# Optimization experiments

Hardware: AMD Instinct MI355X
Metric: run time of the kernel (lower is better)

The kernel has to match this reference:

```python
import jax, jax.numpy as jnp
import numpy as np

N_EMBD = 1024
N_HEAD = 16
DIM_HEAD = N_EMBD // N_HEAD
SCALE = DIM_HEAD ** (-0.5)  # source divides by this (i.e. multiplies scores by sqrt(dim_head))


def setup_inputs() -> dict:
    key = jax.random.key(0)
    k1, k2, k3, k4, k5 = jax.random.split(key, 5)
    B, Tq, Tkv = 2, 2048, 2048
    x_q = jax.random.normal(k1, (B, Tq, N_EMBD), dtype=jnp.float32)
    x_kv = jax.random.normal(k2, (B, Tkv, N_EMBD), dtype=jnp.float32)
    s = 0.02
    W_q = jax.random.normal(k3, (N_EMBD, N_EMBD), dtype=jnp.float32) * s
    W_kv = jax.random.normal(k4, (N_EMBD, 2 * N_EMBD), dtype=jnp.float32) * s
    W_proj = jax.random.normal(k5, (N_EMBD, N_EMBD), dtype=jnp.float32) * s
    return {"x_q": x_q, "x_kv": x_kv, "W_q": W_q, "W_kv": W_kv, "W_proj": W_proj}


def reference(x_q, x_kv, W_q, W_kv, W_proj):
    B, Tq, C = x_q.shape
    Tkv = x_kv.shape[1]
    q = x_q @ W_q                      # [B, Tq, C]
    kv = x_kv @ W_kv                   # [B, Tkv, 2C]
    k, v = jnp.split(kv, 2, axis=2)
    # [B, H, T, Dh]
    q = q.reshape(B, Tq, N_HEAD, DIM_HEAD).transpose(0, 2, 1, 3)
    k = k.reshape(B, Tkv, N_HEAD, DIM_HEAD).transpose(0, 2, 1, 3)
    v = v.reshape(B, Tkv, N_HEAD, DIM_HEAD).transpose(0, 2, 1, 3)
    # Faithful to source: scores = q@k^T / scale  (== * sqrt(dim_head))
    attn = jnp.einsum('bhqd,bhkd->bhqk', q, k) / SCALE
    attn = jax.nn.softmax(attn, axis=-1)
    y = jnp.einsum('bhqk,bhkd->bhqd', attn, v)
    y = y.transpose(0, 2, 1, 3).reshape(B, Tq, C)
    return y @ W_proj
```

## Files before the change

kernel.cpp:

```cpp
#include <hip/hip_runtime.h>
#include <cstddef>

typedef _Float16 f16;
typedef _Float16 f16x8 __attribute__((ext_vector_type(8)));
typedef _Float16 f16x4 __attribute__((ext_vector_type(4)));
typedef _Float16 f16x2 __attribute__((ext_vector_type(2)));
typedef float f32x4 __attribute__((ext_vector_type(4)));
typedef float f32x16 __attribute__((ext_vector_type(16)));
typedef unsigned int u32;

__device__ inline float exp2_fast(float x) {
  float r;
  asm("v_exp_f32 %0, %1" : "=v"(r) : "v"(x));
  return r;
}

__device__ inline int pk2(float x, float y) {
  return __builtin_bit_cast(int, __builtin_amdgcn_cvt_pkrtz(x, y));
}

__device__ inline f16x2 pk2h(float x, float y) {
  return __builtin_bit_cast(f16x2, __builtin_amdgcn_cvt_pkrtz(x, y));
}

__device__ inline void permlane32_swap(int& a, int& b) {
  asm volatile("v_permlane32_swap_b32 %0, %1" : "+v"(a), "+v"(b));
}

__global__ __launch_bounds__(256) void prep(
    const float* __restrict__ xq, const float* __restrict__ xkv,
    f16* __restrict__ oq, f16* __restrict__ okv,
    const float* __restrict__ Wq, const float* __restrict__ Wkv,
    const float* __restrict__ Wp, f16* __restrict__ Wqt,
    f16* __restrict__ Wkvt, f16* __restrict__ Wpt) {
  __shared__ float t[32][33];
  int bid = blockIdx.x;
  if (bid < 8192) {
    const float* in = (bid < 4096) ? xq : xkv;
    f16* out = (bid < 4096) ? oq : okv;
    int i = ((bid & 4095) * 256 + threadIdx.x) * 4;
    float4 v = *(const float4*)&in[i];
    f16x4 h;
    h[0] = (f16)v.x; h[1] = (f16)v.y; h[2] = (f16)v.z; h[3] = (f16)v.w;
    *(f16x4*)&out[i] = h;
  } else {
    int zz = bid - 8192;
    int bx = zz & 31, by = (zz >> 5) & 31, z = zz >> 10;
    const float* in;
    f16* out;
    int N = 1024, extra = 0;
    if (z == 0) { in = Wq; out = Wqt; }
    else if (z == 3) { in = Wp; out = Wpt; }
    else { in = Wkv; out = Wkvt; N = 2048; extra = (z - 1) * 1024; }
    int tx = threadIdx.x % 32, ty = threadIdx.x / 32;
    int n0 = bx * 32 + extra, k0 = by * 32;
#pragma unroll
    for (int i = 0; i < 32; i += 8)
      t[ty + i][tx] = in[(size_t)(k0 + ty + i) * N + n0 + tx];
    __syncthreads();
#pragma unroll
    for (int i = 0; i < 32; i += 8)
      out[(size_t)(n0 + ty + i) * 1024 + k0 + tx] = (f16)t[tx][ty + i];
  }
}

template <int BN, typename CT>
__device__ __forceinline__ void gemm_body(
    const f16* __restrict__ A, const f16* __restrict__ Bt, CT* __restrict__ C,
    int bid, int M, int N, int K, float scale, f16* As, f16* Bs) {
  constexpr int NT = BN / 32;
  constexpr int BI = BN / 32;
  const int nb = N / BN;
  const int m0 = (bid / nb) * 128;
  const int n0 = (bid % nb) * BN;
  const int tid = threadIdx.x;
  const int w = tid >> 6, lane = tid & 63;
  const int l16 = lane & 15, quad = lane >> 4;
  const int wrow = (w >> 1) * 64, wcol = (w & 1) * (BN / 2);
  const int sr = tid >> 3, sc8 = tid & 7;
  const int wc8 = sc8 ^ (sr & 7);

  f32x4 acc[4][NT] = {};
  f16x8 ar[4], br[BI];

#pragma unroll
  for (int i = 0; i < 4; i++)
    ar[i] = *(const f16x8*)&A[(size_t)(m0 + sr + i * 32) * K + sc8 * 8];
#pragma unroll
  for (int i = 0; i < BI; i++)
    br[i] = *(const f16x8*)&Bt[(size_t)(n0 + sr + i * 32) * K + sc8 * 8];

  for (int k0 = 0; k0 < K; k0 += 64) {
#pragma unroll
    for (int i = 0; i < 4; i++)
      *(f16x8*)&As[(sr + i * 32) * 64 + wc8 * 8] = ar[i];
#pragma unroll
    for (int i = 0; i < BI; i++)
      *(f16x8*)&Bs[(sr + i * 32) * 64 + wc8 * 8] = br[i];
    __syncthreads();

    if (k0 + 64 < K) {
#pragma unroll
      for (int i = 0; i < 4; i++)
        ar[i] = *(const f16x8*)&A[(size_t)(m0 + sr + i * 32) * K + k0 + 64 + sc8 * 8];
#pragma unroll
      for (int i = 0; i < BI; i++)
        br[i] = *(const f16x8*)&Bt[(size_t)(n0 + sr + i * 32) * K + k0 + 64 + sc8 * 8];
    }

    f16x8 bf[NT][2];
#pragma unroll
    for (int nt = 0; nt < NT; nt++) {
      const int row = wcol + nt * 16 + l16;
#pragma unroll
      for (int s = 0; s < 2; s++)
        bf[nt][s] = *(const f16x8*)&Bs[row * 64 + (((s * 4 + quad) ^ (row & 7)) << 3)];
    }
#pragma unroll
    for (int mt = 0; mt < 4; mt++) {
      const int row = wrow + mt * 16 + l16;
      f16x8 af0 = *(const f16x8*)&As[row * 64 + ((quad ^ (row & 7)) << 3)];
      f16x8 af1 = *(const f16x8*)&As[row * 64 + (((4 + quad) ^ (row & 7)) << 3)];
#pragma unroll
      for (int nt = 0; nt < NT; nt++) {
        acc[mt][nt] = __builtin_amdgcn_mfma_f32_16x16x32_f16(af0, bf[nt][0], acc[mt][nt], 0, 0, 0);
        acc[mt][nt] = __builtin_amdgcn_mfma_f32_16x16x32_f16(af1, bf[nt][1], acc[mt][nt], 0, 0, 0);
      }
    }
    __syncthreads();
  }

#pragma unroll
  for (int mt = 0; mt < 4; mt++)
#pragma unroll
    for (int nt = 0; nt < NT; nt++)
#pragma unroll
      for (int r = 0; r < 4; r++) {
        int row = m0 + wrow + mt * 16 + quad * 4 + r;
        int col = n0 + wcol + nt * 16 + l16;
        C[(size_t)row * N + col] = (CT)(acc[mt][nt][r] * scale);
      }
}

__global__ __launch_bounds__(256, 3) void qkv_gemm(
    const f16* __restrict__ Xq, const f16* __restrict__ Wqt, f16* __restrict__ Qh,
    const f16* __restrict__ Xkv, const f16* __restrict__ Wkvt, f16* __restrict__ KVh,
    float sc_q) {
  __shared__ f16 As[128 * 64];
  __shared__ f16 Bs[128 * 64];
  if (blockIdx.x < 256)
    gemm_body<128, f16>(Xq, Wqt, Qh, blockIdx.x, 4096, 1024, 1024, sc_q, As, Bs);
  else
    gemm_body<128, f16>(Xkv, Wkvt, KVh, blockIdx.x - 256, 4096, 2048, 1024, 1.0f, As, Bs);
}

template <int BN, typename CT>
__global__ __launch_bounds__(256, 2) void gemm_lds(
    const f16* __restrict__ A, const f16* __restrict__ Bt, CT* __restrict__ C,
    int M, int N, int K, float scale) {
  __shared__ f16 As[128 * 64];
  __shared__ f16 Bs[BN * 64];
  gemm_body<BN, CT>(A, Bt, C, blockIdx.x, M, N, K, scale, As, Bs);
}

__global__ __launch_bounds__(256) void attn_kernel(
    const f16* __restrict__ Qh, const f16* __restrict__ KVh, f16* __restrict__ Yh) {
  __shared__ f16 smem[9216];
  f16* Ks = smem;
  f16* Vt = smem + 64 * 72;

  const int bid = blockIdx.x;
  const int hb = bid & 31;
  const int qt = bid >> 5;
  const int h = hb >> 1, b = hb & 1;
  const int tid = threadIdx.x;
  const int w = tid >> 6, lane = tid & 63;
  const int l31 = lane & 31, e = lane >> 5;

  const size_t qrow0 = (size_t)b * 2048 + (size_t)qt * 128;
  const size_t kvrow0 = (size_t)b * 2048;

  f16x8 qf[4];
#pragma unroll
  for (int ks = 0; ks < 4; ks++)
    qf[ks] = *(const f16x8*)&Qh[(qrow0 + w * 32 + l31) * 1024 + h * 64 + ks * 16 + e * 8];

  float m_run = -1e30f, l_run = 0.0f;
  f32x16 o_acc[2] = {};

  const int ksr = tid >> 2, ksc = (tid & 3) << 4;
  const int vkv0 = (tid >> 3) * 2;
  const int vd0 = (tid & 7) * 8;
  const int vcol = ((((vkv0 >> 3) ^ (tid & 7)) << 3) | (vkv0 & 7));

  f16x8 kr0, kr1, vr0, vr1;
  {
    const f16* kb = &KVh[(kvrow0 + ksr) * 2048 + h * 64 + ksc];
    kr0 = *(const f16x8*)kb;
    kr1 = *(const f16x8*)(kb + 8);
    const f16* vb = &KVh[(kvrow0 + vkv0) * 2048 + 1024 + h * 64 + vd0];
    vr0 = *(const f16x8*)vb;
    vr1 = *(const f16x8*)(vb + 2048);
  }

  for (int t = 0; t < 32; t++) {
    *(f16x8*)&Ks[ksr * 72 + ksc] = kr0;
    *(f16x8*)&Ks[ksr * 72 + ksc + 8] = kr1;
#pragma unroll
    for (int j = 0; j < 8; j++) {
      f16x2 p; p[0] = vr0[j]; p[1] = vr1[j];
      *(f16x2*)&Vt[(vd0 + j) * 72 + vcol] = p;
    }
    __syncthreads();

    if (t + 1 < 32) {
      const f16* kb = &KVh[(kvrow0 + (t + 1) * 64 + ksr) * 2048 + h * 64 + ksc];
      kr0 = *(const f16x8*)kb;
      kr1 = *(const f16x8*)(kb + 8);
      const f16* vb = &KVh[(kvrow0 + (t + 1) * 64 + vkv0) * 2048 + 1024 + h * 64 + vd0];
      vr0 = *(const f16x8*)vb;
      vr1 = *(const f16x8*)(vb + 2048);
    }

    f32x16 sacc[2] = {};
#pragma unroll
    for (int kvt = 0; kvt < 2; kvt++)
#pragma unroll
      for (int ks = 0; ks < 4; ks++) {
        f16x8 a = *(const f16x8*)&Ks[(kvt * 32 + l31) * 72 + ks * 16 + e * 8];
        sacc[kvt] = __builtin_amdgcn_mfma_f32_32x32x16_f16(a, qf[ks], sacc[kvt], 0, 0, 0);
      }

    float mxa[4];
#pragma unroll
    for (int j = 0; j < 4; j++) {
      float a = fmaxf(fmaxf(sacc[0][j], sacc[0][j + 4]),
                      fmaxf(sacc[0][j + 8], sacc[0][j + 12]));
      float bb = fmaxf(fmaxf(sacc[1][j], sacc[1][j + 4]),
                       fmaxf(sacc[1][j + 8], sacc[1][j + 12]));
      mxa[j] = fmaxf(a, bb);
    }
    float mx = fmaxf(fmaxf(mxa[0], mxa[1]), fmaxf(mxa[2], mxa[3]));
    mx = fmaxf(mx, __shfl_xor(mx, 32, 64));

    if (!__all(mx <= m_run + 8.0f)) {
      float mnew = fmaxf(m_run, mx);
      float alpha = exp2_fast(m_run - mnew);
      m_run = mnew;
      l_run *= alpha;
#pragma unroll
      for (int r = 0; r < 16; r++) { o_acc[0][r] *= alpha; o_acc[1][r] *= alpha; }
    }

    float ss0 = 0.0f, ss1 = 0.0f, ss2 = 0.0f, ss3 = 0.0f;
#pragma unroll
    for (int kvt = 0; kvt < 2; kvt++)
#pragma unroll
      for (int r = 0; r < 16; r += 4) {
        float p0 = exp2_fast(sacc[kvt][r + 0] - m_run);
        float p1 = exp2_fast(sacc[kvt][r + 1] - m_run);
        float p2 = exp2_fast(sacc[kvt][r + 2] - m_run);
        float p3 = exp2_fast(sacc[kvt][r + 3] - m_run);
        sacc[kvt][r + 0] = p0; sacc[kvt][r + 1] = p1;
        sacc[kvt][r + 2] = p2; sacc[kvt][r + 3] = p3;
        ss0 += p0; ss1 += p1; ss2 += p2; ss3 += p3;
      }
    float ssum = (ss0 + ss1) + (ss2 + ss3);
    ssum += __shfl_xor(ssum, 32, 64);
    l_run += ssum;

    f16x8 pf[4];
#pragma unroll
    for (int kvt = 0; kvt < 2; kvt++)
#pragma unroll
      for (int half = 0; half < 2; half++) {
        const int h8 = half * 8;
        int a0 = pk2(sacc[kvt][h8 + 0], sacc[kvt][h8 + 1]);
        int b0 = pk2(sacc[kvt][h8 + 4], sacc[kvt][h8 + 5]);
        int a1 = pk2(sacc[kvt][h8 + 2], sacc[kvt][h8 + 3]);
        int b1 = pk2(sacc[kvt][h8 + 6], sacc[kvt][h8 + 7]);
        permlane32_swap(a0, b0);
        permlane32_swap(a1, b1);
        union { int i[4]; f16x8 v; } u;
        u.i[0] = a0; u.i[1] = a1; u.i[2] = b0; u.i[3] = b1;
        pf[kvt * 2 + half] = u.v;
      }

#pragma unroll
    for (int dt = 0; dt < 2; dt++) {
      const int d = dt * 32 + l31;
      const int dx = d >> 3;
#pragma unroll
      for (int ks = 0; ks < 4; ks++) {
        f16x8 va = *(const f16x8*)&Vt[d * 72 + (((ks * 2 + e) ^ dx) << 3)];
        o_acc[dt] = __builtin_amdgcn_mfma_f32_32x32x16_f16(va, pf[ks], o_acc[dt], 0, 0, 0);
      }
    }
    __syncthreads();
  }

  float linv = 1.0f / l_run;
  f16* Of = smem + w * 32 * 72;
#pragma unroll
  for (int dt = 0; dt < 2; dt++)
#pragma unroll
    for (int r2 = 0; r2 < 4; r2++) {
      f16x2 h0 = pk2h(o_acc[dt][r2 * 4 + 0] * linv, o_acc[dt][r2 * 4 + 1] * linv);
      f16x2 h1 = pk2h(o_acc[dt][r2 * 4 + 2] * linv, o_acc[dt][r2 * 4 + 3] * linv);
      f16x4 hh; hh[0] = h0[0]; hh[1] = h0[1]; hh[2] = h1[0]; hh[3] = h1[1];
      *(f16x4*)&Of[l31 * 72 + dt * 32 + r2 * 8 + e * 4] = hh;
    }
  const int qq = lane >> 1, dh = (lane & 1) * 32;
#pragma unroll
  for (int j = 0; j < 4; j++) {
    f16x8 v = *(const f16x8*)&Of[qq * 72 + dh + j * 8];
    *(f16x8*)&Yh[(qrow0 + w * 32 + qq) * 1024 + h * 64 + dh + j * 8] = v;
  }
}

extern "C" void kernel_launch(void* const* d_in, const int* in_sizes, int n_in,
                              void* d_out, int out_size, void* d_ws, size_t ws_size,
                              hipStream_t stream) {
  const float* x_q  = (const float*)d_in[0];
  const float* x_kv = (const float*)d_in[1];
  const float* W_q  = (const float*)d_in[2];
  const float* W_kv = (const float*)d_in[3];
  const float* W_p  = (const float*)d_in[4];
  float* out = (float*)d_out;

  f16* Wq_t  = (f16*)d_ws;
  f16* Wkv_t = Wq_t  + (size_t)1024 * 1024;
  f16* Wp_t  = Wkv_t + (size_t)2048 * 1024;
  f16* Qh    = Wp_t  + (size_t)1024 * 1024;
  f16* KVh   = Qh    + (size_t)4096 * 1024;
  f16* Yh    = KVh   + (size_t)4096 * 2048;
  f16* Xq_h  = Yh;
  f16* Xkv_h = Yh    + (size_t)4096 * 1024;

  prep<<<12288, 256, 0, stream>>>(x_q, x_kv, Xq_h, Xkv_h,
                                  W_q, W_kv, W_p, Wq_t, Wkv_t, Wp_t);

  const float SC = 11.5415603f;
  qkv_gemm<<<768, 256, 0, stream>>>(Xq_h, Wq_t, Qh, Xkv_h, Wkv_t, KVh, SC);

  attn_kernel<<<512, 256, 0, stream>>>(Qh, KVh, Yh);

  gemm_lds<64, float><<<512, 256, 0, stream>>>(Yh, Wp_t, out, 4096, 1024, 1024, 1.0f);
}
```

Measured before the change: 207.1 us.

## Split attention KV range across two wave groups and merge softmax partials

The attention block grows from 256 to 512 threads. Two groups of four waves each process half of the KV sequence for the same 128 query rows, each with its own K/V staging buffers in LDS. At the end, half 1 writes its partial output and max/sum stats to LDS, and half 0 combines them with a log-sum-exp merge before storing. The aim is to halve the serial KV loop length per block and raise the number of waves in flight. The cost is double the LDS, extra barriers, an fp32 merge step, and each block reading Q twice.

```diff
diff --git a/kernel.cpp b/kernel.cpp
--- a/kernel.cpp
+++ b/kernel.cpp
@@ -163,11 +163,9 @@
   gemm_body<BN, CT>(A, Bt, C, blockIdx.x, M, N, K, scale, As, Bs);
 }
 
-__global__ __launch_bounds__(256) void attn_kernel(
+__global__ __launch_bounds__(512, 4) void attn_kernel(
     const f16* __restrict__ Qh, const f16* __restrict__ KVh, f16* __restrict__ Yh) {
-  __shared__ f16 smem[9216];
-  f16* Ks = smem;
-  f16* Vt = smem + 64 * 72;
+  __shared__ f16 smem[18432];
 
   const int bid = blockIdx.x;
   const int hb = bid & 31;
@@ -176,22 +174,27 @@
   const int tid = threadIdx.x;
   const int w = tid >> 6, lane = tid & 63;
   const int l31 = lane & 31, e = lane >> 5;
+  const int qw = w & 3, half = w >> 2;
+  const int tl = tid & 255;
+
+  f16* Ks = smem + half * (2 * 64 * 72);
+  f16* Vt = Ks + 64 * 72;
 
   const size_t qrow0 = (size_t)b * 2048 + (size_t)qt * 128;
-  const size_t kvrow0 = (size_t)b * 2048;
+  const size_t kvrow0 = (size_t)b * 2048 + (size_t)half * 1024;
 
   f16x8 qf[4];
 #pragma unroll
   for (int ks = 0; ks < 4; ks++)
-    qf[ks] = *(const f16x8*)&Qh[(qrow0 + w * 32 + l31) * 1024 + h * 64 + ks * 16 + e * 8];
+    qf[ks] = *(const f16x8*)&Qh[(qrow0 + qw * 32 + l31) * 1024 + h * 64 + ks * 16 + e * 8];
 
   float m_run = -1e30f, l_run = 0.0f;
   f32x16 o_acc[2] = {};
 
-  const int ksr = tid >> 2, ksc = (tid & 3) << 4;
-  const int vkv0 = (tid >> 3) * 2;
-  const int vd0 = (tid & 7) * 8;
-  const int vcol = ((((vkv0 >> 3) ^ (tid & 7)) << 3) | (vkv0 & 7));
+  const int ksr = tl >> 2, ksc = (tl & 3) << 4;
+  const int vkv0 = (tl >> 3) * 2;
+  const int vd0 = (tl & 7) * 8;
+  const int vcol = ((((vkv0 >> 3) ^ (tl & 7)) << 3) | (vkv0 & 7));
 
   f16x8 kr0, kr1, vr0, vr1;
   {
@@ -203,7 +206,7 @@
     vr1 = *(const f16x8*)(vb + 2048);
   }
 
-  for (int t = 0; t < 32; t++) {
+  for (int t = 0; t < 16; t++) {
     *(f16x8*)&Ks[ksr * 72 + ksc] = kr0;
     *(f16x8*)&Ks[ksr * 72 + ksc + 8] = kr1;
 #pragma unroll
@@ -213,7 +216,7 @@
     }
     __syncthreads();
 
-    if (t + 1 < 32) {
+    if (t + 1 < 16) {
       const f16* kb = &KVh[(kvrow0 + (t + 1) * 64 + ksr) * 2048 + h * 64 + ksc];
       kr0 = *(const f16x8*)kb;
       kr1 = *(const f16x8*)(kb + 8);
@@ -273,8 +276,8 @@
 #pragma unroll
     for (int kvt = 0; kvt < 2; kvt++)
 #pragma unroll
-      for (int half = 0; half < 2; half++) {
-        const int h8 = half * 8;
+      for (int hf = 0; hf < 2; hf++) {
+        const int h8 = hf * 8;
         int a0 = pk2(sacc[kvt][h8 + 0], sacc[kvt][h8 + 1]);
         int b0 = pk2(sacc[kvt][h8 + 4], sacc[kvt][h8 + 5]);
         int a1 = pk2(sacc[kvt][h8 + 2], sacc[kvt][h8 + 3]);
@@ -283,7 +286,7 @@
         permlane32_swap(a1, b1);
         union { int i[4]; f16x8 v; } u;
         u.i[0] = a0; u.i[1] = a1; u.i[2] = b0; u.i[3] = b1;
-        pf[kvt * 2 + half] = u.v;
+        pf[kvt * 2 + hf] = u.v;
       }
 
 #pragma unroll
@@ -299,22 +302,59 @@
     __syncthreads();
   }
 
-  float linv = 1.0f / l_run;
-  f16* Of = smem + w * 32 * 72;
-#pragma unroll
-  for (int dt = 0; dt < 2; dt++)
-#pragma unroll
-    for (int r2 = 0; r2 < 4; r2++) {
-      f16x2 h0 = pk2h(o_acc[dt][r2 * 4 + 0] * linv, o_acc[dt][r2 * 4 + 1] * linv);
-      f16x2 h1 = pk2h(o_acc[dt][r2 * 4 + 2] * linv, o_acc[dt][r2 * 4 + 3] * linv);
-      f16x4 hh; hh[0] = h0[0]; hh[1] = h0[1]; hh[2] = h1[0]; hh[3] = h1[1];
-      *(f16x4*)&Of[l31 * 72 + dt * 32 + r2 * 8 + e * 4] = hh;
-    }
-  const int qq = lane >> 1, dh = (lane & 1) * 32;
-#pragma unroll
-  for (int j = 0; j < 4; j++) {
-    f16x8 v = *(const f16x8*)&Of[qq * 72 + dh + j * 8];
-    *(f16x8*)&Yh[(qrow0 + w * 32 + qq) * 1024 + h * 64 + dh + j * 8] = v;
+  float* Om = (float*)smem;
+  float* ML = (float*)smem + 4 * 32 * 68;
+  if (half == 1) {
+#pragma unroll
+    for (int dt = 0; dt < 2; dt++)
+#pragma unroll
+      for (int r2 = 0; r2 < 4; r2++) {
+        f32x4 vv;
+        vv[0] = o_acc[dt][r2 * 4 + 0];
+        vv[1] = o_acc[dt][r2 * 4 + 1];
+        vv[2] = o_acc[dt][r2 * 4 + 2];
+        vv[3] = o_acc[dt][r2 * 4 + 3];
+        *(f32x4*)&Om[(qw * 32 + l31) * 68 + dt * 32 + r2 * 8 + e * 4] = vv;
+      }
+    ML[qw * 64 + l31] = m_run;
+    ML[qw * 64 + 32 + l31] = l_run;
+  }
+  __syncthreads();
+  float linv = 0.0f;
+  if (half == 0) {
+    float m1 = ML[qw * 64 + l31], l1 = ML[qw * 64 + 32 + l31];
+    float mm = fmaxf(m_run, m1);
+    float a0 = exp2_fast(m_run - mm), a1 = exp2_fast(m1 - mm);
+    linv = 1.0f / (l_run * a0 + l1 * a1);
+#pragma unroll
+    for (int dt = 0; dt < 2; dt++)
+#pragma unroll
+      for (int r2 = 0; r2 < 4; r2++) {
+        f32x4 o1 = *(const f32x4*)&Om[(qw * 32 + l31) * 68 + dt * 32 + r2 * 8 + e * 4];
+#pragma unroll
+        for (int j = 0; j < 4; j++)
+          o_acc[dt][r2 * 4 + j] = o_acc[dt][r2 * 4 + j] * a0 + o1[j] * a1;
+      }
+  }
+  __syncthreads();
+
+  if (half == 0) {
+    f16* Of = smem + qw * 32 * 72;
+#pragma unroll
+    for (int dt = 0; dt < 2; dt++)
+#pragma unroll
+      for (int r2 = 0; r2 < 4; r2++) {
+        f16x2 h0 = pk2h(o_acc[dt][r2 * 4 + 0] * linv, o_acc[dt][r2 * 4 + 1] * linv);
+        f16x2 h1 = pk2h(o_acc[dt][r2 * 4 + 2] * linv, o_acc[dt][r2 * 4 + 3] * linv);
+        f16x4 hh; hh[0] = h0[0]; hh[1] = h0[1]; hh[2] = h1[0]; hh[3] = h1[1];
+        *(f16x4*)&Of[l31 * 72 + dt * 32 + r2 * 8 + e * 4] = hh;
+      }
+    const int qq = lane >> 1, dh = (lane & 1) * 32;
+#pragma unroll
+    for (int j = 0; j < 4; j++) {
+      f16x8 v = *(const f16x8*)&Of[qq * 72 + dh + j * 8];
+      *(f16x8*)&Yh[(qrow0 + qw * 32 + qq) * 1024 + h * 64 + dh + j * 8] = v;
+    }
   }
 }
 
@@ -343,7 +383,7 @@
   const float SC = 11.5415603f;
   qkv_gemm<<<768, 256, 0, stream>>>(Xq_h, Wq_t, Qh, Xkv_h, Wkv_t, KVh, SC);
 
-  attn_kernel<<<512, 256, 0, stream>>>(Qh, KVh, Yh);
+  attn_kernel<<<512, 512, 0, stream>>>(Qh, KVh, Yh);
 
   gemm_lds<64, float><<<512, 256, 0, stream>>>(Yh, Wp_t, out, 4096, 1024, 1024, 1.0f);
 }
```

Result: no change. 203.9 us (-1.6%).
